# Performance work log

Measured on AMD Instinct MI355X. Metric: run time of the kernel, lower is better.

## Reference

```python
import jax, jax.numpy as jnp
import numpy as np

SELECT_NUM = 5
N_OBJ = 256


def conv(x, w, b, stride=1, pad=None):
    """NCHW conv. pad=None -> VALID; pad=1 -> [(1,1),(1,1)]."""
    padding = 'VALID' if pad is None else [(pad, pad), (pad, pad)]
    out = jax.lax.conv_general_dilated(
        x, w, (stride, stride), padding,
        dimension_numbers=('NCHW', 'OIHW', 'NCHW'))
    return out + b[None, :, None, None]


def setup_inputs() -> dict:
    key = jax.random.key(0)
    ks = jax.random.split(key, 20)

    def p(k, shape, fan_in):
        return (jax.random.normal(k, shape, jnp.float32) / np.float32(np.sqrt(fan_in)))

    inp = {}
    inp['glob_feature'] = jax.random.normal(ks[0], (1, 1024, 28, 28), jnp.float32)
    inp['roi_features'] = jax.random.normal(ks[1], (N_OBJ, 2048, 7, 7), jnp.float32)
    # valid boxes in a 1280x720 image: x1>x0, y1>y0 so log(.) is finite
    x0 = jax.random.uniform(ks[2], (N_OBJ,), minval=0.0, maxval=600.0)
    y0 = jax.random.uniform(ks[3], (N_OBJ,), minval=0.0, maxval=340.0)
    x1 = x0 + jax.random.uniform(ks[4], (N_OBJ,), minval=10.0, maxval=600.0)
    y1 = y0 + jax.random.uniform(ks[5], (N_OBJ,), minval=10.0, maxval=340.0)
    inp['bbox'] = jnp.stack([x0, y0, x1, y1], axis=1)

    # global branch
    inp['w_glob1'] = p(ks[6], (512, 1024, 4, 4), 1024 * 16); inp['b_glob1'] = jnp.zeros(512, jnp.float32)
    inp['w_glob2'] = p(ks[7], (256, 512, 4, 4), 512 * 16);   inp['b_glob2'] = jnp.zeros(256, jnp.float32)
    # object branch
    inp['w_obj1'] = p(ks[8], (1024, 2048, 3, 3), 2048 * 9);  inp['b_obj1'] = jnp.zeros(1024, jnp.float32)
    inp['w_obj2'] = p(ks[9], (256, 1024, 3, 3), 1024 * 9);   inp['b_obj2'] = jnp.zeros(256, jnp.float32)
    # selector (516 = 260 obj + 256 glob)
    inp['w_sel1'] = p(ks[10], (256, 516, 3, 3), 516 * 9);    inp['b_sel1'] = jnp.zeros(256, jnp.float32)
    inp['w_sel2'] = p(ks[11], (16, 256, 3, 3), 256 * 9);     inp['b_sel2'] = jnp.zeros(16, jnp.float32)
    inp['w_sel3'] = p(ks[12], (1, 16, 3, 3), 16 * 9);        inp['b_sel3'] = jnp.zeros(1, jnp.float32)
    # FC head (eval mode: dropout = identity)
    inp['w_fc1'] = p(ks[13], (516, 256), 516);               inp['b_fc1'] = jnp.zeros(256, jnp.float32)
    inp['w_fc2'] = p(ks[14], (256 * SELECT_NUM, 64), 1280);  inp['b_fc2'] = jnp.zeros(64, jnp.float32)
    inp['w_fc3'] = p(ks[15], (64, 4), 64);                   inp['b_fc3'] = jnp.zeros(4, jnp.float32)
    return inp


def reference(glob_feature, roi_features, bbox,
              w_glob1, b_glob1, w_glob2, b_glob2,
              w_obj1, b_obj1, w_obj2, b_obj2,
              w_sel1, b_sel1, w_sel2, b_sel2, w_sel3, b_sel3,
              w_fc1, b_fc1, w_fc2, b_fc2, w_fc3, b_fc3):
    # global branch: [1,1024,28,28] -> [1,512,14,14] -> [1,256,7,7]; pool(7) is identity
    glob = jax.nn.relu(conv(glob_feature, w_glob1, b_glob1, stride=2, pad=1))
    glob = jax.nn.relu(conv(glob, w_glob2, b_glob2, stride=2, pad=1))

    # object branch: [N,2048,7,7] -> [N,1024,7,7] -> [N,256,7,7]
    obj = jax.nn.relu(conv(roi_features, w_obj1, b_obj1, pad=1))
    obj = jax.nn.relu(conv(obj, w_obj2, b_obj2, pad=1))

    # bbox normalization (uses original coords; image is 1280x720)
    x0, y0, x1, y1 = bbox[:, 0], bbox[:, 1], bbox[:, 2], bbox[:, 3]
    bb = jnp.stack([x0 / 1280.0, y0 / 720.0,
                    jnp.log(1280.0 / (x1 - x0)),
                    jnp.log(720.0 / (y1 - y0))], axis=1)  # [N,4]
    bb = jnp.broadcast_to(bb[:, :, None, None], (bb.shape[0], 4, 7, 7))
    obj = jnp.concatenate([bb, obj], axis=1)  # [N,260,7,7]

    # selector: concat with broadcast glob, 3 valid convs 7->5->3->1
    glob2 = jnp.broadcast_to(glob, (obj.shape[0], 256, 7, 7))
    s = jnp.concatenate([obj, glob2], axis=1)  # [N,516,7,7]
    s = jax.nn.relu(conv(s, w_sel1, b_sel1))
    s = jax.nn.relu(conv(s, w_sel2, b_sel2))
    s = conv(s, w_sel3, b_sel3).reshape(-1)  # [N]

    # top-k selection (sort descending over objects)
    idx = jnp.argsort(-s)[:SELECT_NUM]
    obj = obj[idx] / np.float32(SELECT_NUM)  # [5,260,7,7]

    # adaptive avg pool to 1x1 == mean over HW
    obj = obj.mean(axis=(2, 3))                               # [5,260]
    g = jnp.broadcast_to(glob.mean(axis=(2, 3)), (SELECT_NUM, 256))  # [5,256]
    x = jnp.concatenate([obj, g], axis=1)                     # [5,516]

    x = jax.nn.relu(x @ w_fc1 + b_fc1)   # dropout is identity in eval
    tmp = x.reshape(-1)                  # [1280]
    x = jax.nn.relu(tmp @ w_fc2 + b_fc2) # [64]
    x = x @ w_fc3 + b_fc3                # [4]
    return x
```

## Files before the change

kernel.cpp:

```cpp
#include <hip/hip_runtime.h>
#include <math.h>

using half8 = __attribute__((ext_vector_type(8))) _Float16;
using half4 = __attribute__((ext_vector_type(4))) _Float16;
using f32x4 = __attribute__((ext_vector_type(4))) float;

template<int CIN, int KC, int M_, int BM>
__device__ void transform_w_dev(float* lds, const float* __restrict__ w,
                                _Float16* __restrict__ wt, int s, int m0, int tid) {
  constexpr int NT = (KC / 32) * 9;
  const int ci0 = s * 32;
  int vlen = (CIN - ci0) * 9;
  if (vlen > 288) vlen = 288;
  if (vlen < 0) vlen = 0;
  for (int e = tid; e < 32 * 288; e += 256) {
    const int mi = e / 288, o = e - mi * 288;
    float v = 0.f;
    if (o < vlen) v = w[(size_t)(m0 + mi) * (CIN * 9) + (size_t)ci0 * 9 + o];
    lds[mi * 289 + o] = v;
  }
  __syncthreads();
  const int cc = s >> 2, sub = s & 3;
  int ns = (KC - 128 * cc) / 32; if (ns > 4) ns = 4;
  const int mt = m0 / BM;
  const int mb = m0 - mt * BM;
  _Float16* base = wt + (size_t)mt * NT * (BM * 32);
  for (int u = tid; u < 36 * 256; u += 256) {
    const int chunk = u >> 8, within = u & 255;
    const int g = chunk & 3, khkw = chunk >> 2;
    const int mi = within >> 3, i = within & 7;
    const int kt = 36 * cc + khkw * ns + sub;
    const float v = lds[mi * 289 + (8 * g + i) * 9 + khkw];
    base[(size_t)kt * (BM * 32) + g * (BM * 8) + (mb + mi) * 8 + i] = (_Float16)v;
  }
}

__device__ void convert_tr_dev(_Float16 (*t_s)[136], const float* __restrict__ x,
                               _Float16* __restrict__ xh, int cb, int obj, int tid) {
  const int cbase = cb * 128;
  const float* src = x + (size_t)obj * 2048 * 49 + (size_t)cbase * 49;
  for (int e = tid; e < 128 * 49; e += 256) {
    const int ci = e / 49, pos = e - ci * 49;
    t_s[pos][ci] = (_Float16)src[e];
  }
  __syncthreads();
  _Float16* dst = xh + (size_t)obj * 49 * 2048 + cbase;
  for (int u = tid; u < 49 * 16; u += 256) {
    const int pos = u >> 4, l = u & 15;
    *(half8*)&dst[(size_t)pos * 2048 + l * 8] = *(const half8*)&t_s[pos][l * 8];
  }
}

template<int M_, int CIN, int KH, int KW, int H, int W, int OH, int OW,
         int STRIDE, int PAD, int BATCH, int OUTC, int CO_OFF, bool RELU,
         int TM, int TN, int KSPLIT, bool PARTIAL>
__device__ void conv_gemm_dev(char* shraw, const float* __restrict__ A,
                              const float* __restrict__ X,
                              const float* __restrict__ bias,
                              float* __restrict__ out,
                              int n0, int m0, int kz, int t) {
  constexpr int K   = CIN * KH * KW;
  constexpr int N   = BATCH * OH * OW;
  constexpr int BK  = 16;
  constexpr int BM  = 16 * TM;
  constexpr int BN  = 16 * TN;
  constexpr int KCH = K / KSPLIT;

  float (*a_s)[BM] = (float (*)[BM])shraw;
  float (*b_s)[BN] = (float (*)[BN])(shraw + sizeof(float) * BK * BM);

  const int tx = t & 15;
  const int ty = t >> 4;
  constexpr int AQ    = TM / 4;
  constexpr int TPR_A = 4 / AQ;
  const int am = t / TPR_A;
  const int ak = (t % TPR_A) * (4 * AQ);
  constexpr int BQ = TN / 4;
  const int bk = t & 15;
  const int bn = (t >> 4) * TN;

  float acc[TM][TN];
#pragma unroll
  for (int i = 0; i < TM; i++)
#pragma unroll
    for (int j = 0; j < TN; j++) acc[i][j] = 0.f;

  for (int k0 = kz * KCH; k0 < (kz + 1) * KCH; k0 += BK) {
    float4 av[AQ];
#pragma unroll
    for (int q = 0; q < AQ; q++) {
      av[q] = make_float4(0.f, 0.f, 0.f, 0.f);
      const int kq = k0 + ak + 4 * q;
      if ((m0 + am) < M_ && kq < K)
        av[q] = *reinterpret_cast<const float4*>(&A[(m0 + am) * K + kq]);
    }
    float bv[TN];
#pragma unroll
    for (int q = 0; q < TN; q++) bv[q] = 0.f;
    {
      const int kk = k0 + bk;
      if (kk < K) {
        const int ci = kk / (KH * KW);
        const int r  = kk - ci * (KH * KW);
        const int kh = r / KW;
        const int kw = r - kh * KW;
#pragma unroll
        for (int q = 0; q < TN; q++) {
          const int n = n0 + bn + q;
          if (n < N) {
            const int b   = n / (OH * OW);
            const int pos = n - b * (OH * OW);
            const int oh  = pos / OW;
            const int ow  = pos - oh * OW;
            const int ih  = oh * STRIDE - PAD + kh;
            const int iw  = ow * STRIDE - PAD + kw;
            if (ih >= 0 && ih < H && iw >= 0 && iw < W)
              bv[q] = X[((b * CIN + ci) * H + ih) * W + iw];
          }
        }
      }
    }
    __syncthreads();
#pragma unroll
    for (int q = 0; q < AQ; q++) {
      const int kq = ak + 4 * q;
      a_s[kq + 0][am] = av[q].x;
      a_s[kq + 1][am] = av[q].y;
      a_s[kq + 2][am] = av[q].z;
      a_s[kq + 3][am] = av[q].w;
    }
#pragma unroll
    for (int q = 0; q < BQ; q++)
      *reinterpret_cast<float4*>(&b_s[bk][bn + 4 * q]) =
          make_float4(bv[4 * q], bv[4 * q + 1], bv[4 * q + 2], bv[4 * q + 3]);
    __syncthreads();
#pragma unroll
    for (int kk2 = 0; kk2 < BK; kk2++) {
      float a[TM], b[TN];
#pragma unroll
      for (int q = 0; q < AQ; q++)
        *reinterpret_cast<float4*>(&a[4 * q]) =
            *reinterpret_cast<const float4*>(&a_s[kk2][ty * TM + 4 * q]);
#pragma unroll
      for (int q = 0; q < BQ; q++)
        *reinterpret_cast<float4*>(&b[4 * q]) =
            *reinterpret_cast<const float4*>(&b_s[kk2][tx * TN + 4 * q]);
#pragma unroll
      for (int i = 0; i < TM; i++)
#pragma unroll
        for (int j = 0; j < TN; j++)
          acc[i][j] = fmaf(a[i], b[j], acc[i][j]);
    }
  }

#pragma unroll
  for (int i = 0; i < TM; i++) {
    const int m = m0 + ty * TM + i;
    if (m < M_) {
#pragma unroll
      for (int j = 0; j < TN; j++) {
        const int n = n0 + tx * TN + j;
        if (n < N) {
          if (PARTIAL) {
            out[((size_t)kz * M_ + m) * N + n] = acc[i][j];
          } else {
            float v = acc[i][j] + bias[m];
            if (RELU) v = fmaxf(v, 0.f);
            const int b   = n / (OH * OW);
            const int pos = n - b * (OH * OW);
            out[(b * OUTC + CO_OFF + m) * (OH * OW) + pos] = v;
          }
        }
      }
    }
  }
}

template<int M_, int CIN, int KH, int KW, int H, int W, int OH, int OW,
         int STRIDE, int PAD, int BATCH, int OUTC, int CO_OFF, bool RELU,
         int TM, int TN, int KSPLIT, bool PARTIAL>
__global__ __launch_bounds__(256)
void conv_gemm(const float* __restrict__ A, const float* __restrict__ X,
               const float* __restrict__ bias, float* __restrict__ out) {
  __shared__ char sh[16 * (16 * TM + 16 * TN) * 4];
  conv_gemm_dev<M_, CIN, KH, KW, H, W, OH, OW, STRIDE, PAD, BATCH, OUTC, CO_OFF,
                RELU, TM, TN, KSPLIT, PARTIAL>(
      sh, A, X, bias, out, blockIdx.x * 16 * TN, blockIdx.y * 16 * TM,
      blockIdx.z, threadIdx.x);
}

__global__ __launch_bounds__(256)
void prep1(const float* __restrict__ w_obj1, _Float16* __restrict__ wbuf1,
           const float* __restrict__ roi, _Float16* __restrict__ xh1) {
  __shared__ char sh[32 * 289 * 4];
  int b = blockIdx.x;
  if (b < 2048) {
    transform_w_dev<2048, 2048, 1024, 256>((float*)sh, w_obj1, wbuf1,
                                           b & 63, (b >> 6) * 32, threadIdx.x);
  } else {
    b -= 2048;
    convert_tr_dev((_Float16(*)[136])sh, roi, xh1, b & 15, b >> 4, threadIdx.x);
  }
}

__global__ __launch_bounds__(256)
void prep2(const float* __restrict__ w_obj2, _Float16* __restrict__ wbuf2,
           const float* __restrict__ w_sel1, _Float16* __restrict__ wbufs1,
           const float* __restrict__ w_glob1, const float* __restrict__ gfeat,
           float* __restrict__ part1) {
  __shared__ char sh[32 * 289 * 4];
  int b = blockIdx.x;
  if (b < 256) {
    transform_w_dev<1024, 1024, 256, 128>((float*)sh, w_obj2, wbuf2,
                                          b & 31, (b >> 5) * 32, threadIdx.x);
  } else if (b < 392) {
    b -= 256;
    transform_w_dev<516, 544, 256, 128>((float*)sh, w_sel1, wbufs1,
                                        b % 17, (b / 17) * 32, threadIdx.x);
  } else {
    b -= 392;
    conv_gemm_dev<512, 1024, 4, 4, 28, 28, 14, 14, 2, 1, 1, 512, 0, true,
                  4, 4, 16, true>(sh, w_glob1, gfeat, nullptr, part1,
                                  (b & 3) * 64, ((b >> 2) & 7) * 64, b >> 5,
                                  threadIdx.x);
  }
}

template<int KC, int BM, int NW, int OBJS, int FN, int OHW, int PAD, bool TOUT,
         typename OUT_T, int NMT, int MINW>
__global__ __launch_bounds__(NW * 64, MINW)
void conv_u(const _Float16* __restrict__ Wt, const _Float16* __restrict__ X,
            const float* __restrict__ bias, OUT_T* __restrict__ out,
            int outc, int co_off) {
  constexpr int NT    = (KC / 32) * 9;
  constexpr int OPOS  = OHW * OHW;
  constexpr int WM    = BM / NW;
  constexpr int FR    = WM / 16;
  constexpr int NTHR  = NW * 64;
  constexpr int CFULL = KC / 128;
  constexpr int TAIL  = KC - CFULL * 128;
  constexpr int NCH   = CFULL + (TAIL ? 1 : 0);
  constexpr int NOPB  = 256 / OBJS;
  constexpr int NU    = OBJS * 49 * 16;
  constexpr int NV    = (NU + NTHR - 1) / NTHR;
  constexpr int NUT   = OBJS * 49 * 4;
  constexpr int NVT   = (NUT + NTHR - 1) / NTHR;

  __shared__ alignas(16) _Float16 x_s[OBJS][50][136];

  const int tid  = threadIdx.x;
  const int wid  = tid >> 6;
  const int lane = tid & 63;
  const int g    = lane >> 4;
  const int ln   = lane & 15;
  const int wm   = wid * WM;

  const int bid = blockIdx.x;
  const int j = bid & 7, q = bid >> 3;
  constexpr int OPJ = 8 / NMT;
  const int mt  = j / OPJ;
  const int opb = (j % OPJ) * (NOPB / OPJ) + q;

  for (int e = tid; e < OBJS * 136; e += NTHR)
    x_s[e / 136][49][e % 136] = (_Float16)0.f;

  int ohv[FN], owv[FN], objv[FN];
  bool pvv[FN];
#pragma unroll
  for (int f = 0; f < FN; f++) {
    const int p = ln + 16 * f;
    pvv[f] = p < OBJS * OPOS;
    const int ob = pvv[f] ? (p / OPOS) : (OBJS - 1);
    objv[f] = ob;
    const int pp = pvv[f] ? (p - ob * OPOS) : 0;
    ohv[f] = pp / OHW;
    owv[f] = pp % OHW;
  }

  f32x4 acc[FR][FN];
#pragma unroll
  for (int r = 0; r < FR; r++)
#pragma unroll
    for (int f = 0; f < FN; f++) acc[r][f] = (f32x4){0.f, 0.f, 0.f, 0.f};

  const _Float16* Xh = X + (size_t)opb * OBJS * 49 * KC;

  half8 rg[NV];
  auto load_chunk = [&](int cbase, int cw) {
    if (cw == 128) {
#pragma unroll
      for (int v = 0; v < NV; v++) {
        const int u = v * NTHR + tid;
        if (u < NU) {
          const int row = u >> 4, l = u & 15;
          const int o = (row >= 49) ? 1 : 0, pos = row - 49 * o;
          rg[v] = *(const half8*)(Xh + (size_t)(o * 49 + pos) * KC + cbase + l * 8);
        }
      }
    } else {
#pragma unroll
      for (int v = 0; v < NVT; v++) {
        const int u = v * NTHR + tid;
        if (u < NUT) {
          const int row = u >> 2, l = u & 3;
          const int o = (row >= 49) ? 1 : 0, pos = row - 49 * o;
          rg[v] = *(const half8*)(Xh + (size_t)(o * 49 + pos) * KC + cbase + l * 8);
        }
      }
    }
  };
  auto write_chunk = [&](int cw) {
    if (cw == 128) {
#pragma unroll
      for (int v = 0; v < NV; v++) {
        const int u = v * NTHR + tid;
        if (u < NU) {
          const int row = u >> 4, l = u & 15;
          const int o = (row >= 49) ? 1 : 0, pos = row - 49 * o;
          *(half8*)&x_s[o][pos][l * 8] = rg[v];
        }
      }
    } else {
#pragma unroll
      for (int v = 0; v < NVT; v++) {
        const int u = v * NTHR + tid;
        if (u < NUT) {
          const int row = u >> 2, l = u & 3;
          const int o = (row >= 49) ? 1 : 0, pos = row - 49 * o;
          *(half8*)&x_s[o][pos][l * 8] = rg[v];
        }
      }
    }
  };

  const _Float16* ap = Wt + (size_t)mt * NT * (BM * 32) + (g * BM + wm + ln) * 8;
  half8 afA[FR], afB[FR], afC[FR];
#pragma unroll
  for (int r = 0; r < FR; r++) afA[r] = *(const half8*)(ap + r * 128);
  ap += BM * 32;
#pragma unroll
  for (int r = 0; r < FR; r++) afB[r] = *(const half8*)(ap + r * 128);
  ap += BM * 32;

  load_chunk(0, KC < 128 ? KC : 128);

  auto kstep = [&](half8 (&cur)[FR], half8 (&fut)[FR], int subbyte,
                   const int (&boff)[FN]) {
#pragma unroll
    for (int r = 0; r < FR; r++) fut[r] = *(const half8*)(ap + r * 128);
    ap += BM * 32;
    __builtin_amdgcn_s_setprio(1);
    const char* xb = (const char*)(&x_s[0][0][0]) + subbyte;
#pragma unroll
    for (int f = 0; f < FN; f++) {
      const half8 bf = *(const half8*)(xb + boff[f]);
#pragma unroll
      for (int r = 0; r < FR; r++)
        acc[r][f] = __builtin_amdgcn_mfma_f32_16x16x32_f16(cur[r], bf, acc[r][f], 0, 0, 0);
    }
    __builtin_amdgcn_s_setprio(0);
  };

  for (int c = 0; c < NCH; c++) {
    const int cw = (c < CFULL) ? 128 : TAIL;
    asm volatile("s_barrier" ::: "memory");
    write_chunk(cw);
    if (c + 1 < NCH) load_chunk((c + 1) * 128, (c + 1 < CFULL) ? 128 : TAIL);
    asm volatile("s_waitcnt lgkmcnt(0)\n\ts_barrier" ::: "memory");
    if (cw == 128) {
#pragma unroll
      for (int t9 = 0; t9 < 9; t9++) {
        const int kh = t9 / 3, kw = t9 - 3 * (t9 / 3);
        int boff[FN];
#pragma unroll
        for (int f = 0; f < FN; f++) {
          const int ih = ohv[f] + kh - PAD;
          const int iw = owv[f] + kw - PAD;
          bool v = pvv[f];
          if (PAD) v = v && ((unsigned)ih < 7u) && ((unsigned)iw < 7u);
          const int row = v ? (ih * 7 + iw) : 49;
          boff[f] = (objv[f] * 50 * 136 + row * 136) * 2;
        }
#pragma unroll
        for (int s4 = 0; s4 < 4; s4++) {
          const int ph = (t9 * 4 + s4) % 3;
          const int subbyte = (s4 * 32 + 8 * g) * 2;
          if (ph == 0)      kstep(afA, afC, subbyte, boff);
          else if (ph == 1) kstep(afB, afA, subbyte, boff);
          else              kstep(afC, afB, subbyte, boff);
        }
      }
    } else {
#pragma unroll
      for (int t9 = 0; t9 < 9; t9++) {
        const int kh = t9 / 3, kw = t9 - 3 * (t9 / 3);
        int boff[FN];
#pragma unroll
        for (int f = 0; f < FN; f++) {
          const int ih = ohv[f] + kh - PAD;
          const int iw = owv[f] + kw - PAD;
          bool v = pvv[f];
          if (PAD) v = v && ((unsigned)ih < 7u) && ((unsigned)iw < 7u);
          const int row = v ? (ih * 7 + iw) : 49;
          boff[f] = (objv[f] * 50 * 136 + row * 136) * 2;
        }
        const int ph = t9 % 3;
        const int subbyte = (8 * g) * 2;
        if (ph == 0)      kstep(afA, afC, subbyte, boff);
        else if (ph == 1) kstep(afB, afA, subbyte, boff);
        else              kstep(afC, afB, subbyte, boff);
      }
    }
  }

  if constexpr (TOUT) {
    _Float16 (*ot_s)[49][132] = (_Float16 (*)[49][132]) & x_s[0][0][0];
    constexpr int PASSES = BM / 128;
#pragma unroll
    for (int p = 0; p < PASSES; p++) {
      asm volatile("s_waitcnt lgkmcnt(0)\n\ts_barrier" ::: "memory");
      if (wm >= 128 * p && wm < 128 * (p + 1)) {
#pragma unroll
        for (int f = 0; f < FN; f++) {
          if (pvv[f]) {
            const int pos = ohv[f] * OHW + owv[f];
            const int ob  = objv[f];
#pragma unroll
            for (int r = 0; r < FR; r++) {
              const int cl = wm - 128 * p + r * 16 + g * 4;
              half4 h;
#pragma unroll
              for (int e = 0; e < 4; e++)
                h[e] = (_Float16)fmaxf(
                    acc[r][f][e] + bias[mt * BM + wm + r * 16 + g * 4 + e], 0.f);
              *(half4*)&ot_s[ob][pos][cl] = h;
            }
          }
        }
      }
      asm volatile("s_waitcnt lgkmcnt(0)\n\ts_barrier" ::: "memory");
      for (int u = tid; u < OBJS * OPOS * 32; u += NTHR) {
        const int row = u >> 5, l = u & 31;
        const int o = (row >= OPOS) ? 1 : 0, pos = row - OPOS * o;
        const half4 v = *(const half4*)&ot_s[o][pos][l * 4];
        *(half4*)&((_Float16*)out)[((size_t)(opb * OBJS + o) * OPOS + pos) * outc +
                                   co_off + mt * BM + 128 * p + l * 4] = v;
      }
    }
  } else {
#pragma unroll
    for (int f = 0; f < FN; f++) {
      if (pvv[f]) {
        const int pos = ohv[f] * OHW + owv[f];
        const int bo  = opb * OBJS + objv[f];
#pragma unroll
        for (int r = 0; r < FR; r++) {
          const int mrow = mt * BM + wm + r * 16 + g * 4;
#pragma unroll
          for (int e = 0; e < 4; e++) {
            const int m = mrow + e;
            float v = fmaxf(acc[r][f][e] + bias[m], 0.f);
            out[((size_t)bo * outc + co_off + m) * OPOS + pos] = (OUT_T)v;
          }
        }
      }
    }
  }
}

__global__ void reduce_bias_relu(const float* __restrict__ part,
                                 const float* __restrict__ bias,
                                 float* __restrict__ out, int MN, int N, int KS) {
  const int e = blockIdx.x * 256 + threadIdx.x;
  if (e >= MN) return;
  float s = 0.f;
  for (int k = 0; k < KS; k++) s += part[(size_t)k * MN + e];
  s += bias[e / N];
  out[e] = fmaxf(s, 0.f);
}

__global__ __launch_bounds__(256)
void sel2_kernel(const float* __restrict__ x, const float* __restrict__ w,
                 const float* __restrict__ b, float* __restrict__ out) {
  const int wv   = (blockIdx.x * 256 + threadIdx.x) >> 6;
  const int lane = threadIdx.x & 63;
  const int obj  = wv >> 4, co = wv & 15;
  float acc[9];
#pragma unroll
  for (int p = 0; p < 9; p++) acc[p] = 0.f;
  const float* xo = x + (size_t)obj * 256 * 25;
  const float* wo = w + (size_t)co * 2304;
  for (int k = lane; k < 2304; k += 64) {
    const int ci = k / 9, rr = k - 9 * ci;
    const int kh = rr / 3, kw = rr - 3 * kh;
    const float wval = wo[k];
    const float* xc = xo + ci * 25;
#pragma unroll
    for (int oh = 0; oh < 3; oh++)
#pragma unroll
      for (int ow = 0; ow < 3; ow++)
        acc[oh * 3 + ow] = fmaf(xc[(oh + kh) * 5 + (ow + kw)], wval, acc[oh * 3 + ow]);
  }
  const float bv = b[co];
#pragma unroll
  for (int p = 0; p < 9; p++) {
    float v = acc[p];
#pragma unroll
    for (int off = 32; off; off >>= 1) v += __shfl_xor(v, off);
    if (lane == 0) out[(size_t)wv * 9 + p] = fmaxf(v + bv, 0.f);
  }
}

__global__ void prep_sin_t(const float* __restrict__ bbox,
                           const float* __restrict__ glob,
                           _Float16* __restrict__ sint) {
  const int b = blockIdx.x;
  const float x0 = bbox[b * 4 + 0], y0 = bbox[b * 4 + 1];
  const float x1 = bbox[b * 4 + 2], y1 = bbox[b * 4 + 3];
  const float bbv[4] = {x0 / 1280.f, y0 / 720.f,
                        logf(1280.f / (x1 - x0)), logf(720.f / (y1 - y0))};
  _Float16* base = sint + (size_t)b * 49 * 544;
  for (int e = threadIdx.x; e < 49 * 288; e += blockDim.x) {
    const int pos = e / 288, q = e - pos * 288;
    float v; int c;
    if (q < 4)        { v = bbv[q];                   c = q; }
    else if (q < 260) { v = glob[(q - 4) * 49 + pos]; c = q + 256; }
    else              { v = 0.f;                      c = q + 256; }
    base[pos * 544 + c] = (_Float16)v;
  }
}

__global__ __launch_bounds__(512)
void head_kernel(const float* __restrict__ sel2, const float* __restrict__ w3,
                 const float* __restrict__ b3, const _Float16* __restrict__ sint,
                 const float* __restrict__ glob, const float* __restrict__ w1,
                 const float* __restrict__ b1, const float* __restrict__ w2,
                 const float* __restrict__ b2, const float* __restrict__ wf3,
                 const float* __restrict__ bf3, float* __restrict__ out) {
  __shared__ float w3_s[144];
  __shared__ float s_s[256];
  __shared__ int   idx_s[5];
  __shared__ float objsel_s[5 * 260];
  __shared__ float g_s[256];
  __shared__ float x1_s[1280];
  __shared__ float x2_s[64];
  const int t = threadIdx.x;
  if (t < 144) w3_s[t] = w3[t];
  __syncthreads();
  if (t < 256) {
    float acc = b3[0];
    const float* p = sel2 + t * 144;
    for (int k = 0; k < 144; k++) acc += p[k] * w3_s[k];
    s_s[t] = acc;
  } else {
    const int c = t - 256;
    float s = 0.f;
    const float* p = glob + c * 49;
    for (int q = 0; q < 49; q++) s += p[q];
    g_s[c] = s * (1.f / 49.f);
  }
  __syncthreads();
  if (t == 0) {
    for (int i = 0; i < 5; i++) {
      float best = -1e30f; int bi = 0;
      for (int j = 0; j < 256; j++)
        if (s_s[j] > best) { best = s_s[j]; bi = j; }
      idx_s[i] = bi;
      s_s[bi] = -1e30f;
    }
  }
  __syncthreads();
  for (int e = t; e < 5 * 260; e += 512) {
    const int i = e / 260, c = e - 260 * i;
    const _Float16* base = sint + (size_t)idx_s[i] * 49 * 544;
    float s = 0.f;
    for (int p = 0; p < 49; p++) s += (float)base[p * 544 + c];
    objsel_s[e] = s * (1.f / 245.f);
  }
  __syncthreads();
  if (t < 256) {
    float acc[5];
#pragma unroll
    for (int i = 0; i < 5; i++) acc[i] = b1[t];
    for (int k = 0; k < 260; k++) {
      const float wv = w1[k * 256 + t];
#pragma unroll
      for (int i = 0; i < 5; i++) acc[i] = fmaf(objsel_s[i * 260 + k], wv, acc[i]);
    }
    for (int k = 260; k < 516; k++) {
      const float wv = w1[k * 256 + t];
      const float gv = g_s[k - 260];
#pragma unroll
      for (int i = 0; i < 5; i++) acc[i] = fmaf(gv, wv, acc[i]);
    }
#pragma unroll
    for (int i = 0; i < 5; i++) x1_s[i * 256 + t] = fmaxf(acc[i], 0.f);
  }
  __syncthreads();
  if (t < 64) {
    float a = b2[t];
    for (int k = 0; k < 1280; k++) a = fmaf(x1_s[k], w2[k * 64 + t], a);
    x2_s[t] = fmaxf(a, 0.f);
  }
  __syncthreads();
  if (t < 4) {
    float a = bf3[t];
    for (int k = 0; k < 64; k++) a = fmaf(x2_s[k], wf3[k * 4 + t], a);
    out[t] = a;
  }
}

extern "C" void kernel_launch(void* const* d_in, const int* in_sizes, int n_in,
                              void* d_out, int out_size, void* d_ws, size_t ws_size,
                              hipStream_t stream) {
  (void)in_sizes; (void)n_in; (void)out_size; (void)ws_size;
  const float* glob_feature = (const float*)d_in[0];
  const float* roi          = (const float*)d_in[1];
  const float* bbox         = (const float*)d_in[2];
  const float* w_glob1      = (const float*)d_in[3];
  const float* b_glob1      = (const float*)d_in[4];
  const float* w_glob2      = (const float*)d_in[5];
  const float* b_glob2      = (const float*)d_in[6];
  const float* w_obj1       = (const float*)d_in[7];
  const float* b_obj1       = (const float*)d_in[8];
  const float* w_obj2       = (const float*)d_in[9];
  const float* b_obj2       = (const float*)d_in[10];
  const float* w_sel1       = (const float*)d_in[11];
  const float* b_sel1       = (const float*)d_in[12];
  const float* w_sel2       = (const float*)d_in[13];
  const float* b_sel2       = (const float*)d_in[14];
  const float* w_sel3       = (const float*)d_in[15];
  const float* b_sel3       = (const float*)d_in[16];
  const float* w_fc1        = (const float*)d_in[17];
  const float* b_fc1        = (const float*)d_in[18];
  const float* w_fc2        = (const float*)d_in[19];
  const float* b_fc2        = (const float*)d_in[20];
  const float* w_fc3        = (const float*)d_in[21];
  const float* b_fc3        = (const float*)d_in[22];

  float* ws = (float*)d_ws;
  _Float16* xh1     = (_Float16*)(ws);
  _Float16* wbuf1   = (_Float16*)(ws + 12845056);
  _Float16* obj1buf = (_Float16*)(ws + 22282240);
  _Float16* sint    = (_Float16*)(ws);
  _Float16* wbuf2   = (_Float16*)(ws + 3411968);
  _Float16* wbufs1  = (_Float16*)(ws + 4591616);
  float*    sel1buf = ws + 5218304;
  float*    glob1buf= ws + 6856704;
  float*    part1   = ws + 6957056;
  float*    part2   = ws + 8562688;
  float*    sel2buf = ws + 8763392;
  float*    globbuf = ws + 8800256;

  prep1<<<dim3(6144), 256, 0, stream>>>(w_obj1, wbuf1, roi, xh1);
  conv_u<2048, 256, 8, 2, 7, 7, 1, true, _Float16, 4, 4>
      <<<dim3(512), 512, 0, stream>>>(wbuf1, xh1, b_obj1, obj1buf, 1024, 0);
  prep2<<<dim3(904), 256, 0, stream>>>(w_obj2, wbuf2, w_sel1, wbufs1,
                                       w_glob1, glob_feature, part1);
  reduce_bias_relu<<<dim3(392), 256, 0, stream>>>(part1, b_glob1, glob1buf, 100352, 196, 16);
  conv_gemm<256, 512, 4, 4, 14, 14, 7, 7, 2, 1, 1, 256, 0, true, 4, 4, 16, true>
      <<<dim3(1, 4, 16), 256, 0, stream>>>(w_glob2, glob1buf, b_glob2, part2);
  reduce_bias_relu<<<dim3(49), 256, 0, stream>>>(part2, b_glob2, globbuf, 12544, 49, 16);
  prep_sin_t<<<dim3(256), 256, 0, stream>>>(bbox, globbuf, sint);
  conv_u<1024, 128, 4, 1, 4, 7, 1, true, _Float16, 2, 2>
      <<<dim3(512), 256, 0, stream>>>(wbuf2, obj1buf, b_obj2, sint, 544, 4);
  conv_u<544, 128, 4, 1, 2, 5, 0, false, float, 2, 2>
      <<<dim3(512), 256, 0, stream>>>(wbufs1, sint, b_sel1, sel1buf, 256, 0);
  sel2_kernel<<<dim3(1024), 256, 0, stream>>>(sel1buf, w_sel2, b_sel2, sel2buf);
  head_kernel<<<dim3(1), 512, 0, stream>>>(sel2buf, w_sel3, b_sel3, sint,
                                           globbuf, w_fc1, b_fc1, w_fc2, b_fc2,
                                           w_fc3, b_fc3, (float*)d_out);
}
```

Before: 975.6 us.

## Split conv warps by object, deepen weight prefetch, and double-buffer B fragments

Adds an object-paired warp mapping (OPAIR) to the main obj1 conv. Each warp handles one object's 49 positions with FN=4 instead of both objects' 98 positions with FN=7, and covers twice as many output rows. The weight-fragment register ring is generalised to NBUF buffers, with 4 used for the large convs. An optional prefetch path (BFPF) loads the next step's LDS B fragments before issuing the current MFMAs. These aim to hide global and LDS latency in the dominant GEMM, at the cost of more registers, and the launch-bound occupancy for obj1 drops from 4 to 2.

```diff
diff --git a/kernel.cpp b/kernel.cpp
--- a/kernel.cpp
+++ b/kernel.cpp
@@ -227,19 +227,21 @@
 }
 
 template<int KC, int BM, int NW, int OBJS, int FN, int OHW, int PAD, bool TOUT,
-         typename OUT_T, int NMT, int MINW>
+         typename OUT_T, int NMT, int MINW, bool OPAIR, int NBUF, bool BFPF>
 __global__ __launch_bounds__(NW * 64, MINW)
 void conv_u(const _Float16* __restrict__ Wt, const _Float16* __restrict__ X,
             const float* __restrict__ bias, OUT_T* __restrict__ out,
             int outc, int co_off) {
   constexpr int NT    = (KC / 32) * 9;
   constexpr int OPOS  = OHW * OHW;
-  constexpr int WM    = BM / NW;
+  constexpr int WM    = OPAIR ? (BM * OBJS / NW) : (BM / NW);
   constexpr int FR    = WM / 16;
   constexpr int NTHR  = NW * 64;
   constexpr int CFULL = KC / 128;
   constexpr int TAIL  = KC - CFULL * 128;
   constexpr int NCH   = CFULL + (TAIL ? 1 : 0);
+  static_assert(TAIL == 0 || NBUF == 3, "K-tail requires NBUF==3");
+  static_assert(36 % NBUF == 0, "phase continuity");
   constexpr int NOPB  = 256 / OBJS;
   constexpr int NU    = OBJS * 49 * 16;
   constexpr int NV    = (NU + NTHR - 1) / NTHR;
@@ -253,7 +255,13 @@
   const int lane = tid & 63;
   const int g    = lane >> 4;
   const int ln   = lane & 15;
-  const int wm   = wid * WM;
+  int obj_w = 0, wm;
+  if constexpr (OPAIR) {
+    obj_w = wid / (NW / OBJS);
+    wm = (wid % (NW / OBJS)) * WM;
+  } else {
+    wm = wid * WM;
+  }
 
   const int bid = blockIdx.x;
   const int j = bid & 7, q = bid >> 3;
@@ -268,13 +276,22 @@
   bool pvv[FN];
 #pragma unroll
   for (int f = 0; f < FN; f++) {
-    const int p = ln + 16 * f;
-    pvv[f] = p < OBJS * OPOS;
-    const int ob = pvv[f] ? (p / OPOS) : (OBJS - 1);
-    objv[f] = ob;
-    const int pp = pvv[f] ? (p - ob * OPOS) : 0;
-    ohv[f] = pp / OHW;
-    owv[f] = pp % OHW;
+    if constexpr (OPAIR) {
+      const int pos = ln + 16 * f;
+      pvv[f] = pos < OPOS;
+      objv[f] = obj_w;
+      const int pp = pvv[f] ? pos : 0;
+      ohv[f] = pp / OHW;
+      owv[f] = pp % OHW;
+    } else {
+      const int p = ln + 16 * f;
+      pvv[f] = p < OBJS * OPOS;
+      const int ob = pvv[f] ? (p / OPOS) : (OBJS - 1);
+      objv[f] = ob;
+      const int pp = pvv[f] ? (p - ob * OPOS) : 0;
+      ohv[f] = pp / OHW;
+      owv[f] = pp % OHW;
+    }
   }
 
   f32x4 acc[FR][FN];
@@ -333,33 +350,31 @@
     }
   };
 
+  auto calc_boff = [&](int t9, int (&bo)[FN]) {
+    const int kh = t9 / 3, kw = t9 - 3 * (t9 / 3);
+#pragma unroll
+    for (int f = 0; f < FN; f++) {
+      const int ih = ohv[f] + kh - PAD;
+      const int iw = owv[f] + kw - PAD;
+      bool v = pvv[f];
+      if (PAD) v = v && ((unsigned)ih < 7u) && ((unsigned)iw < 7u);
+      const int row = v ? (ih * 7 + iw) : 49;
+      bo[f] = (objv[f] * 50 * 136 + row * 136) * 2;
+    }
+  };
+
   const _Float16* ap = Wt + (size_t)mt * NT * (BM * 32) + (g * BM + wm + ln) * 8;
-  half8 afA[FR], afB[FR], afC[FR];
-#pragma unroll
-  for (int r = 0; r < FR; r++) afA[r] = *(const half8*)(ap + r * 128);
-  ap += BM * 32;
-#pragma unroll
-  for (int r = 0; r < FR; r++) afB[r] = *(const half8*)(ap + r * 128);
-  ap += BM * 32;
+  half8 af[NBUF][FR];
+#pragma unroll
+  for (int b = 0; b < NBUF - 1; b++) {
+#pragma unroll
+    for (int r = 0; r < FR; r++) af[b][r] = *(const half8*)(ap + r * 128);
+    ap += BM * 32;
+  }
 
   load_chunk(0, KC < 128 ? KC : 128);
 
-  auto kstep = [&](half8 (&cur)[FR], half8 (&fut)[FR], int subbyte,
-                   const int (&boff)[FN]) {
-#pragma unroll
-    for (int r = 0; r < FR; r++) fut[r] = *(const half8*)(ap + r * 128);
-    ap += BM * 32;
-    __builtin_amdgcn_s_setprio(1);
-    const char* xb = (const char*)(&x_s[0][0][0]) + subbyte;
-#pragma unroll
-    for (int f = 0; f < FN; f++) {
-      const half8 bf = *(const half8*)(xb + boff[f]);
-#pragma unroll
-      for (int r = 0; r < FR; r++)
-        acc[r][f] = __builtin_amdgcn_mfma_f32_16x16x32_f16(cur[r], bf, acc[r][f], 0, 0, 0);
-    }
-    __builtin_amdgcn_s_setprio(0);
-  };
+  const char* xsbase = (const char*)(&x_s[0][0][0]);
 
   for (int c = 0; c < NCH; c++) {
     const int cw = (c < CFULL) ? 128 : TAIL;
@@ -367,48 +382,100 @@
     write_chunk(cw);
     if (c + 1 < NCH) load_chunk((c + 1) * 128, (c + 1 < CFULL) ? 128 : TAIL);
     asm volatile("s_waitcnt lgkmcnt(0)\n\ts_barrier" ::: "memory");
+
     if (cw == 128) {
+      if constexpr (BFPF) {
+        int boffC[FN];
+        calc_boff(0, boffC);
+        half8 bf[2][FN];
+        {
+          const char* xb = xsbase + (8 * g) * 2;
+#pragma unroll
+          for (int f = 0; f < FN; f++)
+            bf[0][f] = *(const half8*)(xb + boffC[f]);
+        }
+#pragma unroll
+        for (int t9 = 0; t9 < 9; t9++) {
+#pragma unroll
+          for (int s4 = 0; s4 < 4; s4++) {
+            const int t = t9 * 4 + s4;
+#pragma unroll
+            for (int r = 0; r < FR; r++)
+              af[(t + NBUF - 1) % NBUF][r] = *(const half8*)(ap + r * 128);
+            ap += BM * 32;
+            if (t < 35) {
+              if (s4 < 3) {
+                const char* xb = xsbase + ((s4 + 1) * 32 + 8 * g) * 2;
+#pragma unroll
+                for (int f = 0; f < FN; f++)
+                  bf[(t + 1) & 1][f] = *(const half8*)(xb + boffC[f]);
+              } else {
+                int boffN[FN];
+                calc_boff(t9 + 1, boffN);
+                const char* xb = xsbase + (8 * g) * 2;
+#pragma unroll
+                for (int f = 0; f < FN; f++)
+                  bf[(t + 1) & 1][f] = *(const half8*)(xb + boffN[f]);
+#pragma unroll
+                for (int f = 0; f < FN; f++) boffC[f] = boffN[f];
+              }
+            }
+            __builtin_amdgcn_s_setprio(1);
+#pragma unroll
+            for (int f = 0; f < FN; f++)
+#pragma unroll
+              for (int r = 0; r < FR; r++)
+                acc[r][f] = __builtin_amdgcn_mfma_f32_16x16x32_f16(
+                    af[t % NBUF][r], bf[t & 1][f], acc[r][f], 0, 0, 0);
+            __builtin_amdgcn_s_setprio(0);
+          }
+        }
+      } else {
+#pragma unroll
+        for (int t9 = 0; t9 < 9; t9++) {
+          int boff[FN];
+          calc_boff(t9, boff);
+#pragma unroll
+          for (int s4 = 0; s4 < 4; s4++) {
+            const int t = t9 * 4 + s4;
+#pragma unroll
+            for (int r = 0; r < FR; r++)
+              af[(t + NBUF - 1) % NBUF][r] = *(const half8*)(ap + r * 128);
+            ap += BM * 32;
+            __builtin_amdgcn_s_setprio(1);
+            const char* xb = xsbase + (s4 * 32 + 8 * g) * 2;
+#pragma unroll
+            for (int f = 0; f < FN; f++) {
+              const half8 bfv = *(const half8*)(xb + boff[f]);
+#pragma unroll
+              for (int r = 0; r < FR; r++)
+                acc[r][f] = __builtin_amdgcn_mfma_f32_16x16x32_f16(
+                    af[t % NBUF][r], bfv, acc[r][f], 0, 0, 0);
+            }
+            __builtin_amdgcn_s_setprio(0);
+          }
+        }
+      }
+    } else {
 #pragma unroll
       for (int t9 = 0; t9 < 9; t9++) {
-        const int kh = t9 / 3, kw = t9 - 3 * (t9 / 3);
         int boff[FN];
+        calc_boff(t9, boff);
+#pragma unroll
+        for (int r = 0; r < FR; r++)
+          af[(t9 + NBUF - 1) % NBUF][r] = *(const half8*)(ap + r * 128);
+        ap += BM * 32;
+        __builtin_amdgcn_s_setprio(1);
+        const char* xb = xsbase + (8 * g) * 2;
 #pragma unroll
         for (int f = 0; f < FN; f++) {
-          const int ih = ohv[f] + kh - PAD;
-          const int iw = owv[f] + kw - PAD;
-          bool v = pvv[f];
-          if (PAD) v = v && ((unsigned)ih < 7u) && ((unsigned)iw < 7u);
-          const int row = v ? (ih * 7 + iw) : 49;
-          boff[f] = (objv[f] * 50 * 136 + row * 136) * 2;
-        }
-#pragma unroll
-        for (int s4 = 0; s4 < 4; s4++) {
-          const int ph = (t9 * 4 + s4) % 3;
-          const int subbyte = (s4 * 32 + 8 * g) * 2;
-          if (ph == 0)      kstep(afA, afC, subbyte, boff);
-          else if (ph == 1) kstep(afB, afA, subbyte, boff);
-          else              kstep(afC, afB, subbyte, boff);
-        }
-      }
-    } else {
-#pragma unroll
-      for (int t9 = 0; t9 < 9; t9++) {
-        const int kh = t9 / 3, kw = t9 - 3 * (t9 / 3);
-        int boff[FN];
-#pragma unroll
-        for (int f = 0; f < FN; f++) {
-          const int ih = ohv[f] + kh - PAD;
-          const int iw = owv[f] + kw - PAD;
-          bool v = pvv[f];
-          if (PAD) v = v && ((unsigned)ih < 7u) && ((unsigned)iw < 7u);
-          const int row = v ? (ih * 7 + iw) : 49;
-          boff[f] = (objv[f] * 50 * 136 + row * 136) * 2;
-        }
-        const int ph = t9 % 3;
-        const int subbyte = (8 * g) * 2;
-        if (ph == 0)      kstep(afA, afC, subbyte, boff);
-        else if (ph == 1) kstep(afB, afA, subbyte, boff);
-        else              kstep(afC, afB, subbyte, boff);
+          const half8 bfv = *(const half8*)(xb + boff[f]);
+#pragma unroll
+          for (int r = 0; r < FR; r++)
+            acc[r][f] = __builtin_amdgcn_mfma_f32_16x16x32_f16(
+                af[t9 % NBUF][r], bfv, acc[r][f], 0, 0, 0);
+        }
+        __builtin_amdgcn_s_setprio(0);
       }
     }
   }
@@ -422,18 +489,34 @@
       if (wm >= 128 * p && wm < 128 * (p + 1)) {
 #pragma unroll
         for (int f = 0; f < FN; f++) {
-          if (pvv[f]) {
-            const int pos = ohv[f] * OHW + owv[f];
-            const int ob  = objv[f];
-#pragma unroll
-            for (int r = 0; r < FR; r++) {
-              const int cl = wm - 128 * p + r * 16 + g * 4;
-              half4 h;
-#pragma unroll
-              for (int e = 0; e < 4; e++)
-                h[e] = (_Float16)fmaxf(
-                    acc[r][f][e] + bias[mt * BM + wm + r * 16 + g * 4 + e], 0.f);
-              *(half4*)&ot_s[ob][pos][cl] = h;
+          if constexpr (OPAIR) {
+            const int pos = ln + 16 * f;
+            if (pos < OPOS) {
+#pragma unroll
+              for (int r = 0; r < FR; r++) {
+                const int cl = wm - 128 * p + r * 16 + g * 4;
+                half4 h;
+#pragma unroll
+                for (int e = 0; e < 4; e++)
+                  h[e] = (_Float16)fmaxf(
+                      acc[r][f][e] + bias[mt * BM + wm + r * 16 + g * 4 + e], 0.f);
+                *(half4*)&ot_s[obj_w][pos][cl] = h;
+              }
+            }
+          } else {
+            if (pvv[f]) {
+              const int pos = ohv[f] * OHW + owv[f];
+              const int ob  = objv[f];
+#pragma unroll
+              for (int r = 0; r < FR; r++) {
+                const int cl = wm - 128 * p + r * 16 + g * 4;
+                half4 h;
+#pragma unroll
+                for (int e = 0; e < 4; e++)
+                  h[e] = (_Float16)fmaxf(
+                      acc[r][f][e] + bias[mt * BM + wm + r * 16 + g * 4 + e], 0.f);
+                *(half4*)&ot_s[ob][pos][cl] = h;
+              }
             }
           }
         }
@@ -450,9 +533,11 @@
   } else {
 #pragma unroll
     for (int f = 0; f < FN; f++) {
-      if (pvv[f]) {
-        const int pos = ohv[f] * OHW + owv[f];
-        const int bo  = opb * OBJS + objv[f];
+      const int pos = OPAIR ? (ln + 16 * f) : (ohv[f] * OHW + owv[f]);
+      const bool ok = OPAIR ? (pos < OPOS) : pvv[f];
+      if (ok) {
+        const int pp = OPAIR ? pos : pos;
+        const int bo = opb * OBJS + objv[f];
 #pragma unroll
         for (int r = 0; r < FR; r++) {
           const int mrow = mt * BM + wm + r * 16 + g * 4;
@@ -460,7 +545,7 @@
           for (int e = 0; e < 4; e++) {
             const int m = mrow + e;
             float v = fmaxf(acc[r][f][e] + bias[m], 0.f);
-            out[((size_t)bo * outc + co_off + m) * OPOS + pos] = (OUT_T)v;
+            out[((size_t)bo * outc + co_off + m) * OPOS + pp] = (OUT_T)v;
           }
         }
       }
@@ -653,7 +738,7 @@
   float*    globbuf = ws + 8800256;
 
   prep1<<<dim3(6144), 256, 0, stream>>>(w_obj1, wbuf1, roi, xh1);
-  conv_u<2048, 256, 8, 2, 7, 7, 1, true, _Float16, 4, 4>
+  conv_u<2048, 256, 8, 2, 4, 7, 1, true, _Float16, 4, 2, true, 4, true>
       <<<dim3(512), 512, 0, stream>>>(wbuf1, xh1, b_obj1, obj1buf, 1024, 0);
   prep2<<<dim3(904), 256, 0, stream>>>(w_obj2, wbuf2, w_sel1, wbufs1,
                                        w_glob1, glob_feature, part1);
@@ -662,9 +747,9 @@
       <<<dim3(1, 4, 16), 256, 0, stream>>>(w_glob2, glob1buf, b_glob2, part2);
   reduce_bias_relu<<<dim3(49), 256, 0, stream>>>(part2, b_glob2, globbuf, 12544, 49, 16);
   prep_sin_t<<<dim3(256), 256, 0, stream>>>(bbox, globbuf, sint);
-  conv_u<1024, 128, 4, 1, 4, 7, 1, true, _Float16, 2, 2>
+  conv_u<1024, 128, 4, 1, 4, 7, 1, true, _Float16, 2, 2, false, 4, true>
       <<<dim3(512), 256, 0, stream>>>(wbuf2, obj1buf, b_obj2, sint, 544, 4);
-  conv_u<544, 128, 4, 1, 2, 5, 0, false, float, 2, 2>
+  conv_u<544, 128, 4, 1, 2, 5, 0, false, float, 2, 2, false, 3, false>
       <<<dim3(512), 256, 0, stream>>>(wbufs1, sint, b_sel1, sel1buf, 256, 0);
   sel2_kernel<<<dim3(1024), 256, 0, stream>>>(sel1buf, w_sel2, b_sel2, sel2buf);
   head_kernel<<<dim3(1), 512, 0, stream>>>(sel2buf, w_sel3, b_sel3, sint,
```

New measurement: 964.8 us. No clear change (-1.1%).
